# Performance work log

Hardware: AMD Instinct MI355X
Metric: run time of the kernel (lower is better)

## Reference

```python
import jax, jax.numpy as jnp
import numpy as np

# iRPE config: ratio=1.9, method='euc', mode='ctx', shared_head=True, skip=1, rpe_on='k'
ALPHA, BETA, GAMMA = 1.9, 3.8, 15.2  # alpha=1*ratio, beta=2*ratio, gamma=8*ratio
NUM_HEADS = 12


def _rp_bucket_euc(height, width, skip):
    """Static relative-position bucket ids (Euclidean method, piecewise index).
    Returns (skip+L, skip+L) int array and num_buckets."""
    coords = np.stack(np.meshgrid(np.arange(height), np.arange(width), indexing='ij'), -1)
    coords = coords.reshape(-1, 2).astype(np.float64)  # (L, 2)
    diff = coords[:, None, :] - coords[None, :, :]      # (L, L, 2)
    dis = np.round(np.sqrt((diff ** 2).sum(-1)))        # (L, L), nonnegative
    # piecewise_index: identity for dis<=alpha, log-spaced (rounded, clipped at beta) beyond
    log_idx = np.minimum(
        np.round(ALPHA + np.log(np.maximum(dis, 1e-9) / ALPHA) / np.log(GAMMA / ALPHA) * (BETA - ALPHA)),
        BETA).astype(np.int64)
    bucket = np.where(dis <= ALPHA, np.round(dis).astype(np.int64), log_idx)
    bucket = bucket - bucket.min()
    nb = 2 * int(BETA) + 1  # 7
    if skip > 0:
        L = height * width
        full = np.full((skip + L, skip + L), nb, dtype=np.int64)  # extra bucket for cls token
        full[skip:, skip:] = bucket
        bucket, nb = full, nb + 1  # nb = 8
    return jnp.asarray(bucket), nb


def setup_inputs() -> dict:
    key = jax.random.key(0)
    ks = jax.random.split(key, 4)
    B, N, C = 8, 1025, 768  # 32x32 patches + 1 cls token
    hd = C // NUM_HEADS
    nb = 2 * int(BETA) + 1 + 1  # 8 buckets (incl. skip bucket)
    return {
        "x": jax.random.normal(ks[0], (B, N, C), jnp.float32),
        "qkv_w": jax.random.normal(ks[1], (3 * C, C), jnp.float32) * 0.02,
        "proj_w": jax.random.normal(ks[2], (C, C), jnp.float32) * 0.02,
        "proj_b": jnp.zeros((C,), jnp.float32),
        "rpe_w": jax.random.normal(ks[3], (hd, nb), jnp.float32) * 0.02,  # shared across heads
    }


def reference(x, qkv_w, proj_w, proj_b, rpe_w):
    B, N, C = x.shape
    H = NUM_HEADS
    hd = C // H
    scale = hd ** -0.5
    n_modalities = 1
    height = int((N // n_modalities) ** 0.5)        # 32 (mask is None path)
    skip = N - n_modalities * height * height       # 1 (cls token)
    rp_bucket, _ = _rp_bucket_euc(height, height, skip)  # (N, N) int, static

    qkv = (x @ qkv_w.T).reshape(B, N, 3, H, hd).transpose(2, 0, 3, 1, 4)  # (3,B,H,N,hd)
    q, k, v = qkv[0] * scale, qkv[1], qkv[2]
    attn = jnp.einsum('bhid,bhjd->bhij', q, k)
    # contextual RPE on keys (shared head): bias[b,h,i,j] = q[b,h,i,:] @ rpe_w[:, bucket[i,j]]
    lookup = jnp.einsum('bhid,dm->bhim', q, rpe_w)                      # (B,H,N,nb)
    bias = jnp.take_along_axis(lookup, rp_bucket[None, None, :, :], axis=3)  # (B,H,N,N)
    attn = jax.nn.softmax(attn + bias, axis=-1)
    out = jnp.einsum('bhij,bhjd->bhid', attn, v)
    out = out.transpose(0, 2, 1, 3).reshape(B, N, C)
    return out @ proj_w.T + proj_b
```

## Files before the change

kernel.cpp:

```cpp
#include <hip/hip_runtime.h>
#include <math.h>

#define B_    8
#define N_    1025
#define H_    12
#define HD_   64
#define C_    768
#define BH_   (B_*H_)
#define NTOK  (B_*N_)
#define SCALE 0.125f
#define NPAD  1092
#define NPADV 1088

#define QKV_ELEMS (BH_*N_*HD_)

#define XB_OFF_B     ((size_t)0)
#define WQKV_OFF_B   (XB_OFF_B + (size_t)NTOK*C_*2)
#define WPROJ_OFF_B  (WQKV_OFF_B + (size_t)3*C_*C_*2)
#define QB_OFF_B     (WPROJ_OFF_B + (size_t)C_*C_*2)
#define KB_OFF_B     (QB_OFF_B + (size_t)QKV_ELEMS*2)
#define AOB_OFF_B    (KB_OFF_B + (size_t)QKV_ELEMS*2)
#define VT_OFF_B     (AOB_OFF_B + (size_t)QKV_ELEMS*2)
#define BUCKET_OFF_B (VT_OFF_B + (size_t)BH_*HD_*NPADV*2)

typedef __attribute__((ext_vector_type(8))) short s8bf;
typedef __attribute__((ext_vector_type(8))) unsigned short u8s;
typedef __attribute__((ext_vector_type(4))) float v4f;
typedef unsigned short ushort_t;

#define GLOAD16(gp, lp) __builtin_amdgcn_global_load_lds( \
    (const __attribute__((address_space(1))) unsigned int*)(gp), \
    (__attribute__((address_space(3))) unsigned int*)(lp), 16, 0, 0)

#define SBAR() do { \
    __builtin_amdgcn_sched_barrier(0); \
    asm volatile("s_barrier" ::: "memory"); \
    __builtin_amdgcn_sched_barrier(0); \
} while (0)

__device__ __forceinline__ unsigned short f2bf(float x) {
    union { float f; unsigned u; } v; v.f = x;
    unsigned r = v.u + 0x7FFFu + ((v.u >> 16) & 1u);
    return (unsigned short)(r >> 16);
}

__global__ void bucket_kernel(unsigned char* __restrict__ bucketT) {
    int tid = blockIdx.x * 256 + threadIdx.x;
    if (tid >= N_ * NPAD) return;
    unsigned ut = (unsigned)tid;
    int j = ut / (unsigned)NPAD, i = ut % (unsigned)NPAD;
    if (i >= N_) i = N_ - 1;
    int bk;
    if (i < 1 || j < 1) {
        bk = 7;
    } else {
        int pi = i - 1, pj = j - 1;
        int dy = (pi >> 5) - (pj >> 5);
        int dx = (pi & 31) - (pj & 31);
        int d2 = dy*dy + dx*dx;
        bk = (d2 == 0) ? 0 : ((d2 <= 2) ? 1 : ((d2 <= 12) ? 2 : 3));
    }
    bucketT[tid] = (unsigned char)bk;
}

__global__ __launch_bounds__(256) void cast_kernel(
        const float* __restrict__ x, const float* __restrict__ w1,
        const float* __restrict__ w2,
        ushort_t* __restrict__ xb, ushort_t* __restrict__ w1b,
        ushort_t* __restrict__ w2b) {
    const int NX = NTOK * C_ / 8, NW1 = 3 * C_ * C_ / 8, NW2 = C_ * C_ / 8;
    int g = blockIdx.x * 256 + threadIdx.x;
    const float* src; ushort_t* dst; int idx;
    if (g < NX)                 { src = x;  dst = xb;  idx = g; }
    else if (g < NX + NW1)      { src = w1; dst = w1b; idx = g - NX; }
    else if (g < NX + NW1 + NW2){ src = w2; dst = w2b; idx = g - NX - NW1; }
    else return;
    size_t off = (size_t)idx * 8;
    float4 a = *(const float4*)(src + off);
    float4 c = *(const float4*)(src + off + 4);
    __align__(16) ushort_t h[8] = {f2bf(a.x), f2bf(a.y), f2bf(a.z), f2bf(a.w),
                                   f2bf(c.x), f2bf(c.y), f2bf(c.z), f2bf(c.w)};
    *(u8s*)(dst + off) = *(u8s*)h;
}

__global__ __launch_bounds__(256) void qkv_kernel(
        const ushort_t* __restrict__ xb, const ushort_t* __restrict__ wb,
        ushort_t* __restrict__ qb, ushort_t* __restrict__ kb, ushort_t* __restrict__ vt) {
    __shared__ __align__(16) ushort_t As0[128*64];
    __shared__ __align__(16) ushort_t Bs0[128*64];
    __shared__ __align__(16) ushort_t As1[128*64];
    __shared__ __align__(16) ushort_t Bs1[128*64];
    const int m0 = blockIdx.x * 128, c0 = blockIdx.y * 128;
    const int t = threadIdx.x;
    const int w = t >> 6, lane = t & 63, lc = lane & 15, lq = lane >> 4;
    const int wm = (w >> 1) * 64, wn = (w & 1) * 64;
    const int srow8 = w * 32 + (lane >> 3);
    const int gsw8  = (((lane & 7) ^ (lane >> 3)) & 7) * 8;

    v4f acc[4][4];
#pragma unroll
    for (int mt = 0; mt < 4; mt++)
#pragma unroll
        for (int nt = 0; nt < 4; nt++) acc[mt][nt] = (v4f){0.f, 0.f, 0.f, 0.f};

    auto STAGE = [&](ushort_t* Ad, ushort_t* Bd, int k0) {
#pragma unroll
        for (int i = 0; i < 4; i++) {
            int row = srow8 + i * 8;
            int m = m0 + row; if (m > NTOK - 1) m = NTOK - 1;
            GLOAD16(xb + (size_t)m * C_ + k0 + gsw8,           &Ad[(w*32 + i*8) * 64]);
            GLOAD16(wb + (size_t)(c0 + row) * C_ + k0 + gsw8,  &Bd[(w*32 + i*8) * 64]);
        }
    };
    auto COMPUTE = [&](const ushort_t* A, const ushort_t* B) {
#pragma unroll
        for (int kk = 0; kk < 64; kk += 32) {
            s8bf af[4], bf[4];
#pragma unroll
            for (int mt = 0; mt < 4; mt++)
                af[mt] = *(const s8bf*)&A[(wm + mt*16 + lc) * 64 + ((((kk>>3) + lq) ^ (lc & 7)) * 8)];
#pragma unroll
            for (int nt = 0; nt < 4; nt++)
                bf[nt] = *(const s8bf*)&B[(wn + nt*16 + lc) * 64 + ((((kk>>3) + lq) ^ (lc & 7)) * 8)];
#pragma unroll
            for (int mt = 0; mt < 4; mt++)
#pragma unroll
                for (int nt = 0; nt < 4; nt++)
                    acc[mt][nt] = __builtin_amdgcn_mfma_f32_16x16x32_bf16(af[mt], bf[nt], acc[mt][nt], 0, 0, 0);
        }
    };

    STAGE(As0, Bs0, 0);
#pragma unroll
    for (int it = 0; it < 6; ++it) {
        const int k0 = it * 128;
        if (k0 + 64 < C_) {
            STAGE(As1, Bs1, k0 + 64);
            asm volatile("s_waitcnt vmcnt(8)" ::: "memory");
        } else {
            asm volatile("s_waitcnt vmcnt(0)" ::: "memory");
        }
        SBAR();
        COMPUTE(As0, Bs0);
        SBAR();
        if (k0 + 128 < C_) {
            STAGE(As0, Bs0, k0 + 128);
            asm volatile("s_waitcnt vmcnt(8)" ::: "memory");
        } else {
            asm volatile("s_waitcnt vmcnt(0)" ::: "memory");
        }
        SBAR();
        COMPUTE(As1, Bs1);
        if (it < 5) SBAR();
    }

#pragma unroll
    for (int mt = 0; mt < 4; mt++) {
#pragma unroll
        for (int r = 0; r < 4; r++) {
            int m = m0 + wm + mt*16 + lq*4 + r;
            if (m >= NTOK) continue;
            unsigned um = (unsigned)m;
            int b = um / (unsigned)N_, n = um % (unsigned)N_;
#pragma unroll
            for (int nt = 0; nt < 4; nt++) {
                int c = c0 + wn + nt*16 + lc;
                int comp = c / C_, rem = c % C_;
                int h = rem >> 6, d0 = rem & 63;
                float val = acc[mt][nt][r] * ((comp == 0) ? SCALE : 1.0f);
                if (comp == 2) {
                    vt[((size_t)((b*H_ + h)*HD_ + d0))*NPADV + n] = f2bf(val);
                } else {
                    ushort_t* dst = (comp == 0) ? qb : kb;
                    dst[((size_t)((b*H_ + h)*N_ + n))*HD_ + d0] = f2bf(val);
                }
            }
        }
    }
}

#define LDT  72
#define LUTS 9

__global__ __launch_bounds__(256) void attn_kernel(
        const ushort_t* __restrict__ qb, const ushort_t* __restrict__ kb,
        const ushort_t* __restrict__ vt, const float* __restrict__ rpe,
        const unsigned char* __restrict__ bucketT, ushort_t* __restrict__ ao) {
    __shared__ __align__(16) ushort_t Ks[64*LDT];
    __shared__ __align__(16) ushort_t Vs[64*LDT];
    __shared__ __align__(16) ushort_t Ps[64*LDT];
    __shared__ float lut[64*LUTS];

    const int bh = blockIdx.x, it = blockIdx.y;
    const int b  = bh / H_, hh = bh % H_;
    const int i0 = it * 64;
    const int t  = threadIdx.x;
    const int w  = t >> 6, lane = t & 63, lc = lane & 15, lq = lane >> 4;
    const int row_w = w * 16;

    const ushort_t* qp = qb + (size_t)bh * N_ * HD_;
    const ushort_t* kp = kb + (size_t)bh * N_ * HD_;
    const ushort_t* vp = vt + (size_t)bh * HD_ * NPADV;

    {
        int row = t >> 2, d0 = (t & 3) * 16;
        int gi = i0 + row;
        u8s h0 = (u8s)0, h1 = (u8s)0;
        if (gi < N_) {
            h0 = *(const u8s*)(qp + (size_t)gi * HD_ + d0);
            h1 = *(const u8s*)(qp + (size_t)gi * HD_ + d0 + 8);
        }
        *(u8s*)&Vs[row*LDT + d0]     = h0;
        *(u8s*)&Vs[row*LDT + d0 + 8] = h1;
    }
    if (t < 64) {
        float4 r0 = *(const float4*)(rpe + t*8);
        float4 r1 = *(const float4*)(rpe + t*8 + 4);
        Ps[0*LDT + t] = f2bf(r0.x); Ps[1*LDT + t] = f2bf(r0.y);
        Ps[2*LDT + t] = f2bf(r0.z); Ps[3*LDT + t] = f2bf(r0.w);
        Ps[4*LDT + t] = f2bf(r1.x); Ps[5*LDT + t] = f2bf(r1.y);
        Ps[6*LDT + t] = f2bf(r1.z); Ps[7*LDT + t] = f2bf(r1.w);
    } else if (t < 128) {
        int idx = t - 64;
        int m = 8 + (idx >> 3), c = (idx & 7) * 8;
        *(u8s*)&Ps[m*LDT + c] = (u8s)0;
    }
    __syncthreads();

    s8bf qf0 = *(s8bf*)&Vs[(row_w + lc)*LDT + lq*8];
    s8bf qf1 = *(s8bf*)&Vs[(row_w + lc)*LDT + 32 + lq*8];

    {
        s8bf rf0 = *(s8bf*)&Ps[lc*LDT + lq*8];
        s8bf rf1 = *(s8bf*)&Ps[lc*LDT + 32 + lq*8];
        v4f la = (v4f){0.f, 0.f, 0.f, 0.f};
        la = __builtin_amdgcn_mfma_f32_16x16x32_bf16(qf0, rf0, la, 0, 0, 0);
        la = __builtin_amdgcn_mfma_f32_16x16x32_bf16(qf1, rf1, la, 0, 0, 0);
        if (lc < 8) {
#pragma unroll
            for (int r = 0; r < 4; r++)
                lut[(row_w + lq*4 + r)*LUTS + lc] = la[r];
        }
    }

    const int srow = t >> 2, sd0 = (t & 3) * 16;
    u8s krg0, krg1, vrg0, vrg1;
    {
        const ushort_t* ks = kp + (size_t)srow * HD_ + sd0;
        krg0 = *(const u8s*)ks; krg1 = *(const u8s*)(ks + 8);
        const ushort_t* vs = vp + (size_t)srow * NPADV + sd0;
        vrg0 = *(const u8s*)vs; vrg1 = *(const u8s*)(vs + 8);
    }
    int myrow = i0 + row_w + lc; if (myrow > N_ - 1) myrow = N_ - 1;
    const unsigned char* bkrow = bucketT + (size_t)myrow * NPAD;
    const int lutbase = (row_w + lc) * LUTS;
    unsigned bk4[4];
#pragma unroll
    for (int t4 = 0; t4 < 4; t4++)
        bk4[t4] = *(const unsigned*)(bkrow + t4*16 + lq*4);

    v4f o[4];
    float lsum = 0.f;
#pragma unroll
    for (int dt = 0; dt < 4; dt++) o[dt] = (v4f){0.f, 0.f, 0.f, 0.f};

    for (int jt = 0; jt < 17; jt++) {
        const int j0 = jt * 64;
        __syncthreads();
        {
            ushort_t* kd = &Ks[srow*LDT + sd0];
            *(u8s*)kd = krg0; *(u8s*)(kd + 8) = krg1;
            ushort_t* vd = &Vs[srow*LDT + sd0];
            *(u8s*)vd = vrg0; *(u8s*)(vd + 8) = vrg1;
        }
        __syncthreads();

        unsigned bk4n[4];
        if (jt < 16) {
            int gj = j0 + 64 + srow; if (gj > N_ - 1) gj = N_ - 1;
            const ushort_t* ks = kp + (size_t)gj * HD_ + sd0;
            krg0 = *(const u8s*)ks; krg1 = *(const u8s*)(ks + 8);
            const ushort_t* vs = vp + (size_t)srow * NPADV + (j0 + 64) + sd0;
            vrg0 = *(const u8s*)vs; vrg1 = *(const u8s*)(vs + 8);
#pragma unroll
            for (int t4 = 0; t4 < 4; t4++)
                bk4n[t4] = *(const unsigned*)(bkrow + j0 + 64 + t4*16 + lq*4);
        }

        v4f acc[4];
#pragma unroll
        for (int t4 = 0; t4 < 4; t4++) acc[t4] = (v4f){0.f, 0.f, 0.f, 0.f};
#pragma unroll
        for (int t4 = 0; t4 < 4; t4++) {
            s8bf kf0 = *(s8bf*)&Ks[(t4*16 + lc)*LDT + lq*8];
            s8bf kf1 = *(s8bf*)&Ks[(t4*16 + lc)*LDT + 32 + lq*8];
            acc[t4] = __builtin_amdgcn_mfma_f32_16x16x32_bf16(kf0, qf0, acc[t4], 0, 0, 0);
            acc[t4] = __builtin_amdgcn_mfma_f32_16x16x32_bf16(kf1, qf1, acc[t4], 0, 0, 0);
        }

        float pp[4][4];
#pragma unroll
        for (int t4 = 0; t4 < 4; t4++) {
#pragma unroll
            for (int r = 0; r < 4; r++) {
                int bk = (bk4[t4] >> (8*r)) & 0xFF;
                float sv = acc[t4][r] + lut[lutbase + bk];
                float p = __expf(sv);
                if (jt == 16 && (t4*16 + lq*4 + r) > 0) p = 0.f;
                lsum += p;
                pp[t4][r] = p;
            }
        }
#pragma unroll
        for (int t4 = 0; t4 < 4; t4++) bk4[t4] = bk4n[t4];

#pragma unroll
        for (int t4 = 0; t4 < 4; t4++) {
            uint2 uu;
            uu.x = (unsigned)f2bf(pp[t4][0]) | ((unsigned)f2bf(pp[t4][1]) << 16);
            uu.y = (unsigned)f2bf(pp[t4][2]) | ((unsigned)f2bf(pp[t4][3]) << 16);
            *(uint2*)&Ps[(row_w + lc)*LDT + t4*16 + lq*4] = uu;
        }

        s8bf pf0 = *(s8bf*)&Ps[(row_w + lc)*LDT + lq*8];
        s8bf pf1 = *(s8bf*)&Ps[(row_w + lc)*LDT + 32 + lq*8];
#pragma unroll
        for (int dt = 0; dt < 4; dt++) {
            s8bf vf0 = *(s8bf*)&Vs[(dt*16 + lc)*LDT + lq*8];
            s8bf vf1 = *(s8bf*)&Vs[(dt*16 + lc)*LDT + 32 + lq*8];
            o[dt] = __builtin_amdgcn_mfma_f32_16x16x32_bf16(pf0, vf0, o[dt], 0, 0, 0);
            o[dt] = __builtin_amdgcn_mfma_f32_16x16x32_bf16(pf1, vf1, o[dt], 0, 0, 0);
        }
    }

    lsum += __shfl_xor(lsum, 16);
    lsum += __shfl_xor(lsum, 32);
    if (lq == 0) lut[(row_w + lc)*LUTS + 8] = lsum;
#pragma unroll
    for (int r = 0; r < 4; r++) {
        int i = i0 + row_w + lq*4 + r;
        if (i < N_) {
            float inv = 1.0f / lut[(row_w + lq*4 + r)*LUTS + 8];
#pragma unroll
            for (int dt = 0; dt < 4; dt++)
                ao[((size_t)(b*N_ + i))*C_ + hh*HD_ + dt*16 + lc] = f2bf(o[dt][r] * inv);
        }
    }
}

__global__ __launch_bounds__(256) void proj_kernel(
        const ushort_t* __restrict__ ab, const ushort_t* __restrict__ wb,
        const float* __restrict__ bias, float* __restrict__ out) {
    __shared__ __align__(16) ushort_t As0[128*64];
    __shared__ __align__(16) ushort_t Bs0[128*64];
    __shared__ __align__(16) ushort_t As1[128*64];
    __shared__ __align__(16) ushort_t Bs1[128*64];
    const int m0 = blockIdx.x * 128, c0 = blockIdx.y * 128;
    const int t = threadIdx.x;
    const int w = t >> 6, lane = t & 63, lc = lane & 15, lq = lane >> 4;
    const int wm = (w >> 1) * 64, wn = (w & 1) * 64;
    const int srow8 = w * 32 + (lane >> 3);
    const int gsw8  = (((lane & 7) ^ (lane >> 3)) & 7) * 8;

    v4f acc[4][4];
#pragma unroll
    for (int mt = 0; mt < 4; mt++)
#pragma unroll
        for (int nt = 0; nt < 4; nt++) acc[mt][nt] = (v4f){0.f, 0.f, 0.f, 0.f};

    auto STAGE = [&](ushort_t* Ad, ushort_t* Bd, int k0) {
#pragma unroll
        for (int i = 0; i < 4; i++) {
            int row = srow8 + i * 8;
            int m = m0 + row; if (m > NTOK - 1) m = NTOK - 1;
            GLOAD16(ab + (size_t)m * C_ + k0 + gsw8,           &Ad[(w*32 + i*8) * 64]);
            GLOAD16(wb + (size_t)(c0 + row) * C_ + k0 + gsw8,  &Bd[(w*32 + i*8) * 64]);
        }
    };
    auto COMPUTE = [&](const ushort_t* A, const ushort_t* B) {
#pragma unroll
        for (int kk = 0; kk < 64; kk += 32) {
            s8bf af[4], bf[4];
#pragma unroll
            for (int mt = 0; mt < 4; mt++)
                af[mt] = *(const s8bf*)&A[(wm + mt*16 + lc) * 64 + ((((kk>>3) + lq) ^ (lc & 7)) * 8)];
#pragma unroll
            for (int nt = 0; nt < 4; nt++)
                bf[nt] = *(const s8bf*)&B[(wn + nt*16 + lc) * 64 + ((((kk>>3) + lq) ^ (lc & 7)) * 8)];
#pragma unroll
            for (int mt = 0; mt < 4; mt++)
#pragma unroll
                for (int nt = 0; nt < 4; nt++)
                    acc[mt][nt] = __builtin_amdgcn_mfma_f32_16x16x32_bf16(af[mt], bf[nt], acc[mt][nt], 0, 0, 0);
        }
    };

    STAGE(As0, Bs0, 0);
#pragma unroll
    for (int it = 0; it < 6; ++it) {
        const int k0 = it * 128;
        if (k0 + 64 < C_) {
            STAGE(As1, Bs1, k0 + 64);
            asm volatile("s_waitcnt vmcnt(8)" ::: "memory");
        } else {
            asm volatile("s_waitcnt vmcnt(0)" ::: "memory");
        }
        SBAR();
        COMPUTE(As0, Bs0);
        SBAR();
        if (k0 + 128 < C_) {
            STAGE(As0, Bs0, k0 + 128);
            asm volatile("s_waitcnt vmcnt(8)" ::: "memory");
        } else {
            asm volatile("s_waitcnt vmcnt(0)" ::: "memory");
        }
        SBAR();
        COMPUTE(As1, Bs1);
        if (it < 5) SBAR();
    }

    float pb[4];
#pragma unroll
    for (int nt = 0; nt < 4; nt++) pb[nt] = bias[c0 + wn + nt*16 + lc];
#pragma unroll
    for (int mt = 0; mt < 4; mt++) {
#pragma unroll
        for (int r = 0; r < 4; r++) {
            int m = m0 + wm + mt*16 + lq*4 + r;
            if (m >= NTOK) continue;
#pragma unroll
            for (int nt = 0; nt < 4; nt++) {
                int c = c0 + wn + nt*16 + lc;
                out[(size_t)m * C_ + c] = acc[mt][nt][r] + pb[nt];
            }
        }
    }
}

extern "C" void kernel_launch(void* const* d_in, const int* in_sizes, int n_in,
                              void* d_out, int out_size, void* d_ws, size_t ws_size,
                              hipStream_t stream) {
    const float* x      = (const float*)d_in[0];
    const float* qkv_w  = (const float*)d_in[1];
    const float* proj_w = (const float*)d_in[2];
    const float* proj_b = (const float*)d_in[3];
    const float* rpe_w  = (const float*)d_in[4];
    float* out = (float*)d_out;

    char* ws = (char*)d_ws;
    ushort_t* xb   = (ushort_t*)(ws + XB_OFF_B);
    ushort_t* wqkv = (ushort_t*)(ws + WQKV_OFF_B);
    ushort_t* wprj = (ushort_t*)(ws + WPROJ_OFF_B);
    ushort_t* qb   = (ushort_t*)(ws + QB_OFF_B);
    ushort_t* kb   = (ushort_t*)(ws + KB_OFF_B);
    ushort_t* aob  = (ushort_t*)(ws + AOB_OFF_B);
    ushort_t* vt   = (ushort_t*)(ws + VT_OFF_B);
    unsigned char* bucketT = (unsigned char*)(ws + BUCKET_OFF_B);

    const int ncast = (NTOK*C_ + 3*C_*C_ + C_*C_) / 8;
    bucket_kernel<<<dim3((N_*NPAD + 255)/256), 256, 0, stream>>>(bucketT);
    cast_kernel<<<dim3((ncast + 255)/256), 256, 0, stream>>>(x, qkv_w, proj_w, xb, wqkv, wprj);
    qkv_kernel<<<dim3(65, 18), 256, 0, stream>>>(xb, wqkv, qb, kb, vt);
    attn_kernel<<<dim3(96, 17), 256, 0, stream>>>(qb, kb, vt, rpe_w, bucketT, aob);
    proj_kernel<<<dim3(65, 6), 256, 0, stream>>>(aob, wprj, proj_b, out);
}
```

Measured before the change: 251.7 us.

## Permute K rows in LDS so P stays in registers for PV MFMA

```diff
diff --git a/kernel.cpp b/kernel.cpp
--- a/kernel.cpp
+++ b/kernel.cpp
@@ -188,7 +188,6 @@
         const unsigned char* __restrict__ bucketT, ushort_t* __restrict__ ao) {
     __shared__ __align__(16) ushort_t Ks[64*LDT];
     __shared__ __align__(16) ushort_t Vs[64*LDT];
-    __shared__ __align__(16) ushort_t Ps[64*LDT];
     __shared__ float lut[64*LUTS];
 
     const int bh = blockIdx.x, it = blockIdx.y;
@@ -216,14 +215,14 @@
     if (t < 64) {
         float4 r0 = *(const float4*)(rpe + t*8);
         float4 r1 = *(const float4*)(rpe + t*8 + 4);
-        Ps[0*LDT + t] = f2bf(r0.x); Ps[1*LDT + t] = f2bf(r0.y);
-        Ps[2*LDT + t] = f2bf(r0.z); Ps[3*LDT + t] = f2bf(r0.w);
-        Ps[4*LDT + t] = f2bf(r1.x); Ps[5*LDT + t] = f2bf(r1.y);
-        Ps[6*LDT + t] = f2bf(r1.z); Ps[7*LDT + t] = f2bf(r1.w);
+        Ks[0*LDT + t] = f2bf(r0.x); Ks[1*LDT + t] = f2bf(r0.y);
+        Ks[2*LDT + t] = f2bf(r0.z); Ks[3*LDT + t] = f2bf(r0.w);
+        Ks[4*LDT + t] = f2bf(r1.x); Ks[5*LDT + t] = f2bf(r1.y);
+        Ks[6*LDT + t] = f2bf(r1.z); Ks[7*LDT + t] = f2bf(r1.w);
     } else if (t < 128) {
         int idx = t - 64;
         int m = 8 + (idx >> 3), c = (idx & 7) * 8;
-        *(u8s*)&Ps[m*LDT + c] = (u8s)0;
+        *(u8s*)&Ks[m*LDT + c] = (u8s)0;
     }
     __syncthreads();
 
@@ -231,8 +230,8 @@
     s8bf qf1 = *(s8bf*)&Vs[(row_w + lc)*LDT + 32 + lq*8];
 
     {
-        s8bf rf0 = *(s8bf*)&Ps[lc*LDT + lq*8];
-        s8bf rf1 = *(s8bf*)&Ps[lc*LDT + 32 + lq*8];
+        s8bf rf0 = *(s8bf*)&Ks[lc*LDT + lq*8];
+        s8bf rf1 = *(s8bf*)&Ks[lc*LDT + 32 + lq*8];
         v4f la = (v4f){0.f, 0.f, 0.f, 0.f};
         la = __builtin_amdgcn_mfma_f32_16x16x32_bf16(qf0, rf0, la, 0, 0, 0);
         la = __builtin_amdgcn_mfma_f32_16x16x32_bf16(qf1, rf1, la, 0, 0, 0);
@@ -244,6 +243,7 @@
     }
 
     const int srow = t >> 2, sd0 = (t & 3) * 16;
+    const int kslot = ((srow >> 5) * 2 + ((srow >> 2) & 1)) * 16 + ((srow >> 3) & 3) * 4 + (srow & 3);
     u8s krg0, krg1, vrg0, vrg1;
     {
         const ushort_t* ks = kp + (size_t)srow * HD_ + sd0;
@@ -254,10 +254,12 @@
     int myrow = i0 + row_w + lc; if (myrow > N_ - 1) myrow = N_ - 1;
     const unsigned char* bkrow = bucketT + (size_t)myrow * NPAD;
     const int lutbase = (row_w + lc) * LUTS;
+    const int jb0 = 8*lq, jb1 = 8*lq + 4, jb2 = 8*lq + 32, jb3 = 8*lq + 36;
     unsigned bk4[4];
-#pragma unroll
-    for (int t4 = 0; t4 < 4; t4++)
-        bk4[t4] = *(const unsigned*)(bkrow + t4*16 + lq*4);
+    bk4[0] = *(const unsigned*)(bkrow + jb0);
+    bk4[1] = *(const unsigned*)(bkrow + jb1);
+    bk4[2] = *(const unsigned*)(bkrow + jb2);
+    bk4[3] = *(const unsigned*)(bkrow + jb3);
 
     v4f o[4];
     float lsum = 0.f;
@@ -268,7 +270,7 @@
         const int j0 = jt * 64;
         __syncthreads();
         {
-            ushort_t* kd = &Ks[srow*LDT + sd0];
+            ushort_t* kd = &Ks[kslot*LDT + sd0];
             *(u8s*)kd = krg0; *(u8s*)(kd + 8) = krg1;
             ushort_t* vd = &Vs[srow*LDT + sd0];
             *(u8s*)vd = vrg0; *(u8s*)(vd + 8) = vrg1;
@@ -282,9 +284,10 @@
             krg0 = *(const u8s*)ks; krg1 = *(const u8s*)(ks + 8);
             const ushort_t* vs = vp + (size_t)srow * NPADV + (j0 + 64) + sd0;
             vrg0 = *(const u8s*)vs; vrg1 = *(const u8s*)(vs + 8);
-#pragma unroll
-            for (int t4 = 0; t4 < 4; t4++)
-                bk4n[t4] = *(const unsigned*)(bkrow + j0 + 64 + t4*16 + lq*4);
+            bk4n[0] = *(const unsigned*)(bkrow + j0 + 64 + jb0);
+            bk4n[1] = *(const unsigned*)(bkrow + j0 + 64 + jb1);
+            bk4n[2] = *(const unsigned*)(bkrow + j0 + 64 + jb2);
+            bk4n[3] = *(const unsigned*)(bkrow + j0 + 64 + jb3);
         }
 
         v4f acc[4];
@@ -299,6 +302,7 @@
         }
 
         float pp[4][4];
+        const int jbs[4] = {jb0, jb1, jb2, jb3};
 #pragma unroll
         for (int t4 = 0; t4 < 4; t4++) {
 #pragma unroll
@@ -306,7 +310,7 @@
                 int bk = (bk4[t4] >> (8*r)) & 0xFF;
                 float sv = acc[t4][r] + lut[lutbase + bk];
                 float p = __expf(sv);
-                if (jt == 16 && (t4*16 + lq*4 + r) > 0) p = 0.f;
+                if (jt == 16 && (jbs[t4] + r) > 0) p = 0.f;
                 lsum += p;
                 pp[t4][r] = p;
             }
@@ -314,16 +318,14 @@
 #pragma unroll
         for (int t4 = 0; t4 < 4; t4++) bk4[t4] = bk4n[t4];
 
-#pragma unroll
-        for (int t4 = 0; t4 < 4; t4++) {
-            uint2 uu;
-            uu.x = (unsigned)f2bf(pp[t4][0]) | ((unsigned)f2bf(pp[t4][1]) << 16);
-            uu.y = (unsigned)f2bf(pp[t4][2]) | ((unsigned)f2bf(pp[t4][3]) << 16);
-            *(uint2*)&Ps[(row_w + lc)*LDT + t4*16 + lq*4] = uu;
-        }
-
-        s8bf pf0 = *(s8bf*)&Ps[(row_w + lc)*LDT + lq*8];
-        s8bf pf1 = *(s8bf*)&Ps[(row_w + lc)*LDT + 32 + lq*8];
+        __align__(16) ushort_t ph[16] = {
+            f2bf(pp[0][0]), f2bf(pp[0][1]), f2bf(pp[0][2]), f2bf(pp[0][3]),
+            f2bf(pp[1][0]), f2bf(pp[1][1]), f2bf(pp[1][2]), f2bf(pp[1][3]),
+            f2bf(pp[2][0]), f2bf(pp[2][1]), f2bf(pp[2][2]), f2bf(pp[2][3]),
+            f2bf(pp[3][0]), f2bf(pp[3][1]), f2bf(pp[3][2]), f2bf(pp[3][3])};
+        s8bf pf0 = *(s8bf*)&ph[0];
+        s8bf pf1 = *(s8bf*)&ph[8];
+
 #pragma unroll
         for (int dt = 0; dt < 4; dt++) {
             s8bf vf0 = *(s8bf*)&Vs[(dt*16 + lc)*LDT + lq*8];
@@ -336,6 +338,7 @@
     lsum += __shfl_xor(lsum, 16);
     lsum += __shfl_xor(lsum, 32);
     if (lq == 0) lut[(row_w + lc)*LUTS + 8] = lsum;
+    __builtin_amdgcn_s_waitcnt(0);
 #pragma unroll
     for (int r = 0; r < 4; r++) {
         int i = i0 + row_w + lq*4 + r;
```

Result: faster. 244.1 us (-3.0%).
